# Kernel tuning notes

Hardware: AMD Instinct MI355X
Metric: run time of the kernel (lower is better)

The kernel has to match this reference:

```python
import jax, jax.numpy as jnp
import numpy as np

B, S, E = 2, 2048, 2048
H, D = 16, 128  # num_heads, head_dim; H*D == E
EPS = 1e-5


def setup_inputs() -> dict:
    key = jax.random.key(0)
    ks = jax.random.split(key, 9)
    s = 0.02
    return {
        "x": jax.random.normal(ks[0], (B, S, E), dtype=jnp.float32),
        "ln1_scale": jnp.ones((E,), dtype=jnp.float32),
        "Wq": jax.random.normal(ks[1], (E, H, D), dtype=jnp.float32) * s,
        "Wk": jax.random.normal(ks[2], (E, H, D), dtype=jnp.float32) * s,
        "Wv": jax.random.normal(ks[3], (E, H, D), dtype=jnp.float32) * s,
        "Wo": jax.random.normal(ks[4], (H, D, E), dtype=jnp.float32) * s,
        "ln2_scale": jnp.ones((E,), dtype=jnp.float32),
        "Wmlp": jax.random.normal(ks[5], (E, E), dtype=jnp.float32) * s,
        "bmlp": jnp.zeros((E,), dtype=jnp.float32),
    }


def _rmsnorm(x, scale, eps=EPS):
    var = jnp.mean(jnp.square(x), axis=-1, keepdims=True)
    return x * jax.lax.rsqrt(var + eps) * scale


def _causal_mha(x, Wq, Wk, Wv, Wo):
    # x: [B,S,E] -> q,k,v: [B,S,H,D]
    q = jnp.einsum("bse,ehd->bshd", x, Wq)
    k = jnp.einsum("bse,ehd->bshd", x, Wk)
    v = jnp.einsum("bse,ehd->bshd", x, Wv)
    scale = 1.0 / jnp.sqrt(jnp.float32(q.shape[-1]))
    scores = jnp.einsum("bqhd,bkhd->bhqk", q, k) * scale  # [B,H,S,S]
    causal = jnp.tril(jnp.ones((x.shape[1], x.shape[1]), dtype=bool))
    scores = jnp.where(causal[None, None], scores, jnp.finfo(scores.dtype).min)
    probs = jax.nn.softmax(scores, axis=-1)
    ctx = jnp.einsum("bhqk,bkhd->bqhd", probs, v)  # [B,S,H,D]
    return jnp.einsum("bqhd,hde->bqe", ctx, Wo)


def reference(x, ln1_scale, Wq, Wk, Wv, Wo, ln2_scale, Wmlp, bmlp):
    # TinyLlamaBlock, schedule[layer_id] == ANCHOR (full causal MHA), use_rope=False
    normed = _rmsnorm(x, ln1_scale)
    attn_out = _causal_mha(normed, Wq, Wk, Wv, Wo)
    x = x + attn_out
    x = x + (_rmsnorm(x, ln2_scale) @ Wmlp + bmlp)
    return x
```

## Files before the change

### kernel.cpp

```cpp
#include <hip/hip_runtime.h>


typedef unsigned short ushort_t;
typedef __attribute__((ext_vector_type(8))) short short8;
typedef __attribute__((ext_vector_type(4))) float floatx4;

__device__ __forceinline__ ushort_t f2bf(float f) {
  union { float f; unsigned u; } v; v.f = f;
  unsigned r = v.u + 0x7fffu + ((v.u >> 16) & 1u);
  return (ushort_t)(r >> 16);
}
__device__ __forceinline__ float bf2f(unsigned h) {
  union { unsigned u; float f; } v; v.u = h << 16; return v.f;
}
__device__ __forceinline__ void load16(const ushort_t* g, ushort_t* l) {
  __builtin_amdgcn_global_load_lds(
      (const __attribute__((address_space(1))) unsigned*)g,
      (__attribute__((address_space(3))) unsigned*)l, 16, 0, 0);
}

__global__ __launch_bounds__(256) void transpose_w_kernel(
    const float* __restrict__ src, ushort_t* __restrict__ dst) {
  __shared__ __align__(16) ushort_t tile[64][72];
  const int t = threadIdx.x;
  const int n0 = blockIdx.x * 64, k0 = blockIdx.y * 64;
#pragma unroll
  for (int i = 0; i < 4; ++i) {
    int c = t + 256 * i;
    int r = c >> 4, o = (c & 15) * 4;
    float4 raw = *(const float4*)&src[(size_t)(k0 + r) * 2048 + n0 + o];
    tile[o + 0][r] = f2bf(raw.x);
    tile[o + 1][r] = f2bf(raw.y);
    tile[o + 2][r] = f2bf(raw.z);
    tile[o + 3][r] = f2bf(raw.w);
  }
  __syncthreads();
#pragma unroll
  for (int i = 0; i < 2; ++i) {
    int c = t + 256 * i;
    int r = c >> 3, o = (c & 7) * 8;
    *(uint4*)&dst[(size_t)(n0 + r) * 2048 + k0 + o] = *(const uint4*)&tile[r][o];
  }
}

template <bool XBF>
__global__ __launch_bounds__(256) void rmsnorm_kernel(
    const void* __restrict__ xv, int in_ld, const float* __restrict__ g,
    ushort_t* __restrict__ out, int out_ld) {
  const int row = blockIdx.x, t = threadIdx.x;
  float v[8];
  if (XBF) {
    uint4 raw = *(const uint4*)((const ushort_t*)xv + (size_t)row * in_ld + t * 8);
    v[0] = bf2f(raw.x & 0xffffu); v[1] = bf2f(raw.x >> 16);
    v[2] = bf2f(raw.y & 0xffffu); v[3] = bf2f(raw.y >> 16);
    v[4] = bf2f(raw.z & 0xffffu); v[5] = bf2f(raw.z >> 16);
    v[6] = bf2f(raw.w & 0xffffu); v[7] = bf2f(raw.w >> 16);
  } else {
    const float* xr = (const float*)xv + (size_t)row * in_ld + t * 8;
    float4 a = *(const float4*)xr;
    float4 b = *(const float4*)(xr + 4);
    v[0] = a.x; v[1] = a.y; v[2] = a.z; v[3] = a.w;
    v[4] = b.x; v[5] = b.y; v[6] = b.z; v[7] = b.w;
  }
  float ss = 0.f;
#pragma unroll
  for (int i = 0; i < 8; ++i) ss += v[i] * v[i];
#pragma unroll
  for (int m = 32; m >= 1; m >>= 1) ss += __shfl_xor(ss, m, 64);
  __shared__ float red[4];
  if ((t & 63) == 0) red[t >> 6] = ss;
  __syncthreads();
  float rs = rsqrtf((red[0] + red[1] + red[2] + red[3]) * (1.0f / 2048.0f) + 1e-5f);
  const float* gp = g + t * 8;
  float4 ga = *(const float4*)gp;
  float4 gb = *(const float4*)(gp + 4);
  float gv[8] = {ga.x, ga.y, ga.z, ga.w, gb.x, gb.y, gb.z, gb.w};
  union { ushort_t u16[8]; uint4 u; } p;
#pragma unroll
  for (int i = 0; i < 8; ++i) p.u16[i] = f2bf(v[i] * rs * gv[i]);
  *(uint4*)&out[(size_t)row * out_ld + t * 8] = p.u;
}

template <int MODE>
__global__ __launch_bounds__(256, 2) void gemm_bt(
    const ushort_t* A, int lda, const ushort_t* Bt, const ushort_t* Bt2,
    int ldb, void* Cv, int ldc, const void* resid, int ldr,
    const float* bias, int M, int N, int K) {
  __shared__ __align__(16) ushort_t As[128][32];
  __shared__ __align__(16) ushort_t Bs[128][32];
  const int t = threadIdx.x;
  const int wid = t >> 6, lane = t & 63;
  const int l15 = lane & 15, quad = lane >> 4;
  const int m0 = blockIdx.y * 128, n0 = blockIdx.x * 128;
  const int wm = (wid >> 1) * 64, wn = (wid & 1) * 64;

  const ushort_t* btb = Bt;
  int nr = n0;
  if (Bt2 != nullptr && n0 >= 4096) { btb = Bt2; nr = n0 - 4096; }

  const int srow = wid * 32 + (lane >> 2);
  const int scol = (lane & 3) * 8;
  const ushort_t* ag0 = &A[(size_t)(m0 + srow) * lda + scol];
  const ushort_t* ag1 = &A[(size_t)(m0 + srow + 16) * lda + scol];
  const ushort_t* bg0 = &btb[(size_t)(nr + srow) * ldb + scol];
  const ushort_t* bg1 = &btb[(size_t)(nr + srow + 16) * ldb + scol];
  ushort_t* al0 = &As[wid * 32][0];
  ushort_t* al1 = &As[wid * 32 + 16][0];
  ushort_t* bl0 = &Bs[wid * 32][0];
  ushort_t* bl1 = &Bs[wid * 32 + 16][0];

  floatx4 acc[4][4];
#pragma unroll
  for (int i = 0; i < 4; ++i)
#pragma unroll
    for (int j = 0; j < 4; ++j) acc[i][j] = (floatx4){0.f, 0.f, 0.f, 0.f};

  for (int k0 = 0; k0 < K; k0 += 32) {
    __syncthreads();
    load16(ag0 + k0, al0);
    load16(ag1 + k0, al1);
    load16(bg0 + k0, bl0);
    load16(bg1 + k0, bl1);
    __syncthreads();

    short8 af[4], bf[4];
#pragma unroll
    for (int i = 0; i < 4; ++i)
      af[i] = *(const short8*)&As[wm + i * 16 + l15][quad * 8];
#pragma unroll
    for (int j = 0; j < 4; ++j)
      bf[j] = *(const short8*)&Bs[wn + j * 16 + l15][quad * 8];
#pragma unroll
    for (int i = 0; i < 4; ++i)
#pragma unroll
      for (int j = 0; j < 4; ++j)
        acc[i][j] = __builtin_amdgcn_mfma_f32_16x16x32_bf16(af[i], bf[j],
                                                            acc[i][j], 0, 0, 0);
  }

#pragma unroll
  for (int i = 0; i < 4; ++i)
#pragma unroll
    for (int j = 0; j < 4; ++j)
#pragma unroll
      for (int r = 0; r < 4; ++r) {
        int row = m0 + wm + i * 16 + quad * 4 + r;
        int col = n0 + wn + j * 16 + l15;
        float v = acc[i][j][r];
        if (MODE == 0) {
          ((ushort_t*)Cv)[(size_t)row * ldc + col] = f2bf(v);
        } else if (MODE == 1) {
          float rv = ((const float*)resid)[(size_t)row * ldr + col];
          ((ushort_t*)Cv)[(size_t)row * ldc + col] = f2bf(rv + v);
        } else {
          float rv = bf2f(((const ushort_t*)resid)[(size_t)row * ldr + col]);
          ((float*)Cv)[(size_t)row * ldc + col] = rv + v + bias[col];
        }
      }
}

__global__ __launch_bounds__(256) void transpose_v_kernel(
    const ushort_t* __restrict__ qkv, ushort_t* __restrict__ vT) {
  __shared__ __align__(16) ushort_t tile[64][72];
  const int t = threadIdx.x;
  const int s0 = blockIdx.x * 64, d0 = blockIdx.y * 64;
  const int bh = blockIdx.z, b = bh >> 4, h = bh & 15;
#pragma unroll
  for (int i = 0; i < 2; ++i) {
    int c = t + 256 * i, r = c >> 3, o = (c & 7) * 8;
    uint4 raw = *(const uint4*)&qkv[(size_t)(b * 2048 + s0 + r) * 6144 + 4096 +
                                    h * 128 + d0 + o];
    tile[o + 0][r] = (ushort_t)(raw.x & 0xffffu);
    tile[o + 1][r] = (ushort_t)(raw.x >> 16);
    tile[o + 2][r] = (ushort_t)(raw.y & 0xffffu);
    tile[o + 3][r] = (ushort_t)(raw.y >> 16);
    tile[o + 4][r] = (ushort_t)(raw.z & 0xffffu);
    tile[o + 5][r] = (ushort_t)(raw.z >> 16);
    tile[o + 6][r] = (ushort_t)(raw.w & 0xffffu);
    tile[o + 7][r] = (ushort_t)(raw.w >> 16);
  }
  __syncthreads();
#pragma unroll
  for (int i = 0; i < 2; ++i) {
    int c = t + 256 * i, r = c >> 3, o = (c & 7) * 8;
    *(uint4*)&vT[((size_t)bh * 128 + d0 + r) * 2048 + s0 + o] =
        *(const uint4*)&tile[r][o];
  }
}

__global__ __launch_bounds__(256, 2) void attn_kernel(
    const ushort_t* qkv, const ushort_t* vT, ushort_t* ctx, int ldctx) {
  const int S = 2048, LD = 6144, D = 128;
  __shared__ __align__(16) ushort_t Ks[2][64][136];
  __shared__ __align__(16) ushort_t Vt[2][128][72];
  __shared__ __align__(16) ushort_t Ps[4][16][72];
  const int t = threadIdx.x;
  const int wid = t >> 6, lane = t & 63;
  const int l15 = lane & 15, quad = lane >> 4;
  const int bx = (int)blockIdx.x;
  const int bh = blockIdx.y, b = bh >> 4, h = bh & 15;

  const int krow = t >> 4, kcol = (t & 15) * 8;
  const int vrow = t >> 3, vcol = (t & 7) * 8;
  const ushort_t* kgp = &qkv[(size_t)(b * S + krow) * LD + 2048 + h * D + kcol];
  const ushort_t* vgp = &vT[((size_t)bh * D + vrow) * S + vcol];

  uint4 k0r, k1r, k2r, k3r, v0r, v1r, v2r, v3r;
#define PREFETCH(KB)                                          \
  do {                                                        \
    const ushort_t* kp_ = kgp + (size_t)(KB)*LD;              \
    k0r = *(const uint4*)(kp_);                               \
    k1r = *(const uint4*)(kp_ + (size_t)16 * LD);             \
    k2r = *(const uint4*)(kp_ + (size_t)32 * LD);             \
    k3r = *(const uint4*)(kp_ + (size_t)48 * LD);             \
    const ushort_t* vp_ = vgp + (KB);                         \
    v0r = *(const uint4*)(vp_);                               \
    v1r = *(const uint4*)(vp_ + (size_t)32 * S);              \
    v2r = *(const uint4*)(vp_ + (size_t)64 * S);              \
    v3r = *(const uint4*)(vp_ + (size_t)96 * S);              \
  } while (0)
#define STAGE(BUF)                                            \
  do {                                                        \
    *(uint4*)&Ks[BUF][krow + 0][kcol]  = k0r;                 \
    *(uint4*)&Ks[BUF][krow + 16][kcol] = k1r;                 \
    *(uint4*)&Ks[BUF][krow + 32][kcol] = k2r;                 \
    *(uint4*)&Ks[BUF][krow + 48][kcol] = k3r;                 \
    *(uint4*)&Vt[BUF][vrow + 0][vcol]  = v0r;                 \
    *(uint4*)&Vt[BUF][vrow + 32][vcol] = v1r;                 \
    *(uint4*)&Vt[BUF][vrow + 64][vcol] = v2r;                 \
    *(uint4*)&Vt[BUF][vrow + 96][vcol] = v3r;                 \
  } while (0)

  const float sc2 = 0.08838834764831845f * 1.4426950408889634f;
  const int nkt0 = 32 - bx;
  const int NT = 33;

  PREFETCH(0);
  STAGE(0);
  PREFETCH(64);

  int g = 0;
  for (int ph = 0; ph < 2; ++ph) {
    const int qtile = ph == 0 ? (31 - bx) : bx;
    const int qb = qtile * 64;

    short8 qf[4];
    {
      const ushort_t* qp =
          &qkv[(size_t)(b * S + qb + wid * 16 + l15) * LD + h * D];
#pragma unroll
      for (int kk = 0; kk < 4; ++kk)
        qf[kk] = *(const short8*)&qp[kk * 32 + quad * 8];
    }

    floatx4 accO[8];
#pragma unroll
    for (int i = 0; i < 8; ++i) accO[i] = (floatx4){0.f, 0.f, 0.f, 0.f};
    float m_i = -1e30f;
    float l_i = 0.f;
    const int qg = qb + wid * 16 + l15;

    const int nkt = qtile + 1;
    for (int kt = 0; kt < nkt; ++kt, ++g) {
      const int kb = kt * 64;
      const int buf = g & 1;
      __syncthreads();
      if (g + 1 < NT) {
        STAGE(buf ^ 1);
        if (g + 2 < NT) {
          const int g2 = g + 2;
          const int kb2 = (g2 < nkt0) ? g2 * 64 : (g2 - nkt0) * 64;
          PREFETCH(kb2);
        }
      }

      floatx4 st[4];
#pragma unroll
      for (int jn = 0; jn < 4; ++jn) {
        st[jn] = (floatx4){0.f, 0.f, 0.f, 0.f};
#pragma unroll
        for (int kk = 0; kk < 4; ++kk) {
          short8 kf = *(const short8*)&Ks[buf][jn * 16 + l15][kk * 32 + quad * 8];
          st[jn] = __builtin_amdgcn_mfma_f32_16x16x32_bf16(kf, qf[kk], st[jn], 0, 0, 0);
        }
      }

      float p[4][4];
      if (kt == nkt - 1) {
#pragma unroll
        for (int jn = 0; jn < 4; ++jn)
#pragma unroll
          for (int r = 0; r < 4; ++r) {
            int kg = kb + jn * 16 + quad * 4 + r;
            float s = st[jn][r] * sc2;
            p[jn][r] = (kg <= qg) ? s : -1e30f;
          }
      } else {
#pragma unroll
        for (int jn = 0; jn < 4; ++jn)
#pragma unroll
          for (int r = 0; r < 4; ++r) p[jn][r] = st[jn][r] * sc2;
      }

      float mq0 = fmaxf(fmaxf(p[0][0], p[0][1]), fmaxf(p[0][2], p[0][3]));
      float mq1 = fmaxf(fmaxf(p[1][0], p[1][1]), fmaxf(p[1][2], p[1][3]));
      float mq2 = fmaxf(fmaxf(p[2][0], p[2][1]), fmaxf(p[2][2], p[2][3]));
      float mq3 = fmaxf(fmaxf(p[3][0], p[3][1]), fmaxf(p[3][2], p[3][3]));
      float v = fmaxf(fmaxf(mq0, mq1), fmaxf(mq2, mq3));
      v = fmaxf(v, __shfl_xor(v, 16, 64));
      v = fmaxf(v, __shfl_xor(v, 32, 64));

      if (!__all(v - m_i <= 8.0f)) {
        float mnew = fmaxf(m_i, v);
        float alpha = exp2f(m_i - mnew);
        m_i = mnew;
        float arow[4];
#pragma unroll
        for (int r = 0; r < 4; ++r) arow[r] = __shfl(alpha, quad * 4 + r, 16);
#pragma unroll
        for (int jd = 0; jd < 8; ++jd)
#pragma unroll
          for (int r = 0; r < 4; ++r) accO[jd][r] *= arow[r];
        l_i *= alpha;
      }

#pragma unroll
      for (int jn = 0; jn < 4; ++jn)
#pragma unroll
        for (int r = 0; r < 4; ++r) p[jn][r] = exp2f(p[jn][r] - m_i);

#pragma unroll
      for (int jn = 0; jn < 4; ++jn) {
        unsigned w0, w1;
        asm("v_cvt_pk_bf16_f32 %0, %1, %2" : "=v"(w0)
            : "v"(p[jn][0]), "v"(p[jn][1]));
        asm("v_cvt_pk_bf16_f32 %0, %1, %2" : "=v"(w1)
            : "v"(p[jn][2]), "v"(p[jn][3]));
        uint2 pk2; pk2.x = w0; pk2.y = w1;
        *(uint2*)&Ps[wid][l15][jn * 16 + quad * 4] = pk2;
      }

      float sq = ((p[0][0] + p[0][1]) + (p[0][2] + p[0][3])) +
                 ((p[1][0] + p[1][1]) + (p[1][2] + p[1][3])) +
                 ((p[2][0] + p[2][1]) + (p[2][2] + p[2][3])) +
                 ((p[3][0] + p[3][1]) + (p[3][2] + p[3][3]));
      sq += __shfl_xor(sq, 16, 64);
      sq += __shfl_xor(sq, 32, 64);
      l_i += sq;

      __asm__ __volatile__("s_waitcnt lgkmcnt(0)" ::: "memory");

      short8 pf[2];
#pragma unroll
      for (int kk = 0; kk < 2; ++kk)
        pf[kk] = *(const short8*)&Ps[wid][l15][kk * 32 + quad * 8];
#pragma unroll
      for (int jd = 0; jd < 8; ++jd)
#pragma unroll
        for (int kk = 0; kk < 2; ++kk) {
          short8 vf = *(const short8*)&Vt[buf][jd * 16 + l15][kk * 32 + quad * 8];
          accO[jd] = __builtin_amdgcn_mfma_f32_16x16x32_bf16(pf[kk], vf, accO[jd], 0, 0, 0);
        }
    }

    float lrow[4];
#pragma unroll
    for (int r = 0; r < 4; ++r) lrow[r] = 1.0f / __shfl(l_i, quad * 4 + r, 16);
#pragma unroll
    for (int jd = 0; jd < 8; ++jd)
#pragma unroll
      for (int r = 0; r < 4; ++r) {
        int row = b * S + qb + wid * 16 + quad * 4 + r;
        int col = h * D + jd * 16 + l15;
        ctx[(size_t)row * ldctx + col] = f2bf(accO[jd][r] * lrow[r]);
      }
  }
#undef PREFETCH
#undef STAGE
}

extern "C" void kernel_launch(void* const* d_in, const int* in_sizes, int n_in,
                              void* d_out, int out_size, void* d_ws,
                              size_t ws_size, hipStream_t stream) {
  const float* x    = (const float*)d_in[0];
  const float* ln1  = (const float*)d_in[1];
  const float* Wq   = (const float*)d_in[2];
  const float* Wk   = (const float*)d_in[3];
  const float* Wv   = (const float*)d_in[4];
  const float* Wo   = (const float*)d_in[5];
  const float* ln2  = (const float*)d_in[6];
  const float* Wmlp = (const float*)d_in[7];
  const float* bmlp = (const float*)d_in[8];
  float* out = (float*)d_out;

  char* ws = (char*)d_ws;
  ushort_t* qkv = (ushort_t*)(ws + 0);
  ushort_t* R2  = (ushort_t*)(ws + 50331648);
  ushort_t* WqT   = R2;
  ushort_t* WkT   = R2 + 4194304;
  ushort_t* vT    = R2;
  ushort_t* WoT   = R2;
  ushort_t* WmlpT = R2;
  ushort_t* n1  = (ushort_t*)d_out;
  ushort_t* WvT = (ushort_t*)d_out + 8388608;
  ushort_t* ctx = qkv + 4096;
  ushort_t* x1  = qkv + 2048;
  ushort_t* n2  = qkv;

  dim3 blk(256);
  dim3 tgrid(32, 32);
  dim3 ggrid(16, 32);
  dim3 ggridQKV(48, 32);

  rmsnorm_kernel<false><<<dim3(4096), blk, 0, stream>>>(x, 2048, ln1, n1, 2048);

  transpose_w_kernel<<<tgrid, blk, 0, stream>>>(Wq, WqT);
  transpose_w_kernel<<<tgrid, blk, 0, stream>>>(Wk, WkT);
  transpose_w_kernel<<<tgrid, blk, 0, stream>>>(Wv, WvT);
  gemm_bt<0><<<ggridQKV, blk, 0, stream>>>(n1, 2048, WqT, WvT, 2048, qkv, 6144,
                                           nullptr, 0, nullptr, 4096, 6144, 2048);

  transpose_v_kernel<<<dim3(32, 2, 32), blk, 0, stream>>>(qkv, vT);

  attn_kernel<<<dim3(16, 32), blk, 0, stream>>>(qkv, vT, ctx, 6144);

  transpose_w_kernel<<<tgrid, blk, 0, stream>>>(Wo, WoT);
  gemm_bt<1><<<ggrid, blk, 0, stream>>>(ctx, 6144, WoT, nullptr, 2048, x1, 6144,
                                        x, 2048, nullptr, 4096, 2048, 2048);

  rmsnorm_kernel<true><<<dim3(4096), blk, 0, stream>>>(x1, 6144, ln2, n2, 6144);

  transpose_w_kernel<<<tgrid, blk, 0, stream>>>(Wmlp, WmlpT);
  gemm_bt<2><<<ggrid, blk, 0, stream>>>(n2, 6144, WmlpT, nullptr, 2048, out, 2048,
                                        x1, 6144, bmlp, 4096, 2048, 2048);
}
```

Measured before the change: 493.1 us.

## Double GEMM K-tile to 64 with XOR-swizzled LDS and batch weight transposes

The GEMM now stages 64-wide K slices per iteration instead of 32. Rows are stored in LDS with an XOR swizzle on the 16-byte chunk index to avoid bank conflicts, and each slice feeds two MFMA sub-steps. This halves the number of barrier pairs per GEMM at the cost of twice the shared memory per block. The weight transposes are merged into two batched launches using blockIdx.z, and workspace buffers are reassigned so the Wo and Wmlp transposes can run earlier, which cuts launch overhead.

Result: faster. 463.5 us (-6.0%).

```diff
diff --git a/kernel.cpp b/kernel.cpp
--- a/kernel.cpp
+++ b/kernel.cpp
@@ -19,9 +19,15 @@
       (__attribute__((address_space(3))) unsigned*)l, 16, 0, 0);
 }
 
-__global__ __launch_bounds__(256) void transpose_w_kernel(
-    const float* __restrict__ src, ushort_t* __restrict__ dst) {
+__global__ __launch_bounds__(256) void transpose_w_batch(
+    const float* __restrict__ s0, const float* __restrict__ s1,
+    const float* __restrict__ s2, ushort_t* __restrict__ d0,
+    ushort_t* __restrict__ d1, ushort_t* __restrict__ d2) {
   __shared__ __align__(16) ushort_t tile[64][72];
+  const float* src = s0;
+  ushort_t* dst = d0;
+  if (blockIdx.z == 1) { src = s1; dst = d1; }
+  else if (blockIdx.z == 2) { src = s2; dst = d2; }
   const int t = threadIdx.x;
   const int n0 = blockIdx.x * 64, k0 = blockIdx.y * 64;
 #pragma unroll
@@ -86,8 +92,8 @@
     const ushort_t* A, int lda, const ushort_t* Bt, const ushort_t* Bt2,
     int ldb, void* Cv, int ldc, const void* resid, int ldr,
     const float* bias, int M, int N, int K) {
-  __shared__ __align__(16) ushort_t As[128][32];
-  __shared__ __align__(16) ushort_t Bs[128][32];
+  __shared__ __align__(16) ushort_t As[128][64];
+  __shared__ __align__(16) ushort_t Bs[128][64];
   const int t = threadIdx.x;
   const int wid = t >> 6, lane = t & 63;
   const int l15 = lane & 15, quad = lane >> 4;
@@ -98,16 +104,12 @@
   int nr = n0;
   if (Bt2 != nullptr && n0 >= 4096) { btb = Bt2; nr = n0 - 4096; }
 
-  const int srow = wid * 32 + (lane >> 2);
-  const int scol = (lane & 3) * 8;
-  const ushort_t* ag0 = &A[(size_t)(m0 + srow) * lda + scol];
-  const ushort_t* ag1 = &A[(size_t)(m0 + srow + 16) * lda + scol];
-  const ushort_t* bg0 = &btb[(size_t)(nr + srow) * ldb + scol];
-  const ushort_t* bg1 = &btb[(size_t)(nr + srow + 16) * ldb + scol];
-  ushort_t* al0 = &As[wid * 32][0];
-  ushort_t* al1 = &As[wid * 32 + 16][0];
-  ushort_t* bl0 = &Bs[wid * 32][0];
-  ushort_t* bl1 = &Bs[wid * 32 + 16][0];
+  const int srow = wid * 8 + (lane >> 3);
+  const int scol = ((lane & 7) ^ ((lane >> 3) & 7)) * 8;
+  const ushort_t* ag = &A[(size_t)(m0 + srow) * lda + scol];
+  const ushort_t* bg = &btb[(size_t)(nr + srow) * ldb + scol];
+  ushort_t* al = &As[wid * 8][0];
+  ushort_t* bl = &Bs[wid * 8][0];
 
   floatx4 acc[4][4];
 #pragma unroll
@@ -115,27 +117,36 @@
 #pragma unroll
     for (int j = 0; j < 4; ++j) acc[i][j] = (floatx4){0.f, 0.f, 0.f, 0.f};
 
-  for (int k0 = 0; k0 < K; k0 += 32) {
+  const char* asb = (const char*)&As[0][0];
+  const char* bsb = (const char*)&Bs[0][0];
+  const int rswz = (l15 & 7);
+
+  for (int k0 = 0; k0 < K; k0 += 64) {
     __syncthreads();
-    load16(ag0 + k0, al0);
-    load16(ag1 + k0, al1);
-    load16(bg0 + k0, bl0);
-    load16(bg1 + k0, bl1);
+#pragma unroll
+    for (int s = 0; s < 4; ++s) {
+      load16(ag + (size_t)(s * 32) * lda + k0, al + s * 32 * 64);
+      load16(bg + (size_t)(s * 32) * ldb + k0, bl + s * 32 * 64);
+    }
     __syncthreads();
 
-    short8 af[4], bf[4];
-#pragma unroll
-    for (int i = 0; i < 4; ++i)
-      af[i] = *(const short8*)&As[wm + i * 16 + l15][quad * 8];
-#pragma unroll
-    for (int j = 0; j < 4; ++j)
-      bf[j] = *(const short8*)&Bs[wn + j * 16 + l15][quad * 8];
-#pragma unroll
-    for (int i = 0; i < 4; ++i)
+#pragma unroll
+    for (int kh = 0; kh < 2; ++kh) {
+      const int gsel = ((kh * 4 + quad) ^ rswz) * 16;
+      short8 af[4], bf[4];
+#pragma unroll
+      for (int i = 0; i < 4; ++i)
+        af[i] = *(const short8*)(asb + (wm + i * 16 + l15) * 128 + gsel);
 #pragma unroll
       for (int j = 0; j < 4; ++j)
-        acc[i][j] = __builtin_amdgcn_mfma_f32_16x16x32_bf16(af[i], bf[j],
-                                                            acc[i][j], 0, 0, 0);
+        bf[j] = *(const short8*)(bsb + (wn + j * 16 + l15) * 128 + gsel);
+#pragma unroll
+      for (int i = 0; i < 4; ++i)
+#pragma unroll
+        for (int j = 0; j < 4; ++j)
+          acc[i][j] = __builtin_amdgcn_mfma_f32_16x16x32_bf16(af[i], bf[j],
+                                                              acc[i][j], 0, 0, 0);
+    }
   }
 
 #pragma unroll
@@ -398,39 +409,38 @@
   ushort_t* R2  = (ushort_t*)(ws + 50331648);
   ushort_t* WqT   = R2;
   ushort_t* WkT   = R2 + 4194304;
-  ushort_t* vT    = R2;
   ushort_t* WoT   = R2;
-  ushort_t* WmlpT = R2;
+  ushort_t* WmlpT = R2 + 4194304;
   ushort_t* n1  = (ushort_t*)d_out;
   ushort_t* WvT = (ushort_t*)d_out + 8388608;
+  ushort_t* vT  = (ushort_t*)d_out + 8388608;
   ushort_t* ctx = qkv + 4096;
   ushort_t* x1  = qkv + 2048;
   ushort_t* n2  = qkv;
 
   dim3 blk(256);
-  dim3 tgrid(32, 32);
   dim3 ggrid(16, 32);
   dim3 ggridQKV(48, 32);
 
   rmsnorm_kernel<false><<<dim3(4096), blk, 0, stream>>>(x, 2048, ln1, n1, 2048);
 
-  transpose_w_kernel<<<tgrid, blk, 0, stream>>>(Wq, WqT);
-  transpose_w_kernel<<<tgrid, blk, 0, stream>>>(Wk, WkT);
-  transpose_w_kernel<<<tgrid, blk, 0, stream>>>(Wv, WvT);
+  transpose_w_batch<<<dim3(32, 32, 3), blk, 0, stream>>>(Wq, Wk, Wv,
+                                                         WqT, WkT, WvT);
   gemm_bt<0><<<ggridQKV, blk, 0, stream>>>(n1, 2048, WqT, WvT, 2048, qkv, 6144,
                                            nullptr, 0, nullptr, 4096, 6144, 2048);
 
+  transpose_w_batch<<<dim3(32, 32, 2), blk, 0, stream>>>(Wo, Wmlp, Wo,
+                                                         WoT, WmlpT, WoT);
+
   transpose_v_kernel<<<dim3(32, 2, 32), blk, 0, stream>>>(qkv, vT);
 
   attn_kernel<<<dim3(16, 32), blk, 0, stream>>>(qkv, vT, ctx, 6144);
 
-  transpose_w_kernel<<<tgrid, blk, 0, stream>>>(Wo, WoT);
   gemm_bt<1><<<ggrid, blk, 0, stream>>>(ctx, 6144, WoT, nullptr, 2048, x1, 6144,
                                         x, 2048, nullptr, 4096, 2048, 2048);
 
   rmsnorm_kernel<true><<<dim3(4096), blk, 0, stream>>>(x1, 6144, ln2, n2, 6144);
 
-  transpose_w_kernel<<<tgrid, blk, 0, stream>>>(Wmlp, WmlpT);
   gemm_bt<2><<<ggrid, blk, 0, stream>>>(n2, 6144, WmlpT, nullptr, 2048, out, 2048,
                                         x1, 6144, bmlp, 4096, 2048, 2048);
 }
```
